# Kernel optimization log

Measured on AMD Instinct MI355X. Metric: run time of the kernel, lower is better.

The kernel has to match this reference:

```python
import jax, jax.numpy as jnp
import numpy as np

H = 1024      # hidden_size
V = 50257     # output_size (vocab)
L = 12        # max_length


def setup_inputs() -> dict:
    key = jax.random.key(0)
    ks = jax.random.split(key, 16)
    s = 0.02  # weight init scale
    return {
        "input_tok": jax.random.randint(ks[0], (1,), 0, V, dtype=jnp.int64) if jax.config.read('jax_enable_x64') else jax.random.randint(ks[0], (1,), 0, V, dtype=jnp.int32),
        "hidden": jax.random.normal(ks[1], (1, 1, H), jnp.float32),
        "encoder_outputs": jax.random.normal(ks[2], (L, H), jnp.float32),
        "emb": jax.random.normal(ks[3], (V, H), jnp.float32) * s,
        "attn_W": jax.random.normal(ks[4], (L, 2 * H), jnp.float32) * s,
        "attn_b": jnp.zeros((L,), jnp.float32),
        "comb_W": jax.random.normal(ks[5], (H, 2 * H), jnp.float32) * s,
        "comb_b": jnp.zeros((H,), jnp.float32),
        "Wih": jax.random.normal(ks[6], (H, H), jnp.float32) * s,
        "Whh": jax.random.normal(ks[7], (H, H), jnp.float32) * s,
        "bih": jnp.zeros((H,), jnp.float32),
        "bhh": jnp.zeros((H,), jnp.float32),
        "out_W": jax.random.normal(ks[8], (V, H), jnp.float32) * s,
        "out_b": jnp.zeros((V,), jnp.float32),
    }


def reference(input_tok, hidden, encoder_outputs, emb, attn_W, attn_b,
              comb_W, comb_b, Wih, Whh, bih, bhh, out_W, out_b):
    # embedding lookup -> [1, H]  (dropout = identity in eval mode)
    embedded = emb[input_tok[0]][None, :]
    h0 = hidden[0]  # [1, H]
    # Bahdanau-style attention over encoder_outputs [L, H]
    attn_in = jnp.concatenate([embedded, h0], axis=1)           # [1, 2H]
    attn_weights = jax.nn.softmax(attn_in @ attn_W.T + attn_b, axis=1)  # [1, L]
    attn_applied = attn_weights @ encoder_outputs               # [1, H]
    # combine + relu
    x = jnp.concatenate([embedded, attn_applied], axis=1)       # [1, 2H]
    x = jax.nn.relu(x @ comb_W.T + comb_b)                      # [1, H]
    # single vanilla-RNN (tanh) step
    h_new = jnp.tanh(x @ Wih.T + bih + h0 @ Whh.T + bhh)        # [1, H]
    # output projection + log_softmax over vocab
    logp = jax.nn.log_softmax(h_new @ out_W.T + out_b, axis=1)  # [1, V]
    return logp, h_new[None, :, :], attn_weights
```

## Files before the change

kernel.cpp:

```cpp
#include <hip/hip_runtime.h>
#include <math.h>

#define H 1024
#define V 50257
#define L 12

#define OFF_EMB    0
#define OFF_ATTN   1024
#define OFF_X      2048
#define OFF_H0     3072
#define OFF_H      4096
#define OFF_LOGITS 5120
#define OFF_PART   56384
#define NB4        4096

__device__ __forceinline__ float dot4(float4 a, float4 b) {
    return a.x * b.x + a.y * b.y + a.z * b.z + a.w * b.w;
}

__device__ __forceinline__ float wave_red(float s) {
    for (int o = 32; o > 0; o >>= 1) s += __shfl_down(s, o);
    return s;
}

__global__ __launch_bounds__(1024) void k1_attn(
    const int* __restrict__ tok_p, const float* __restrict__ hidden,
    const float* __restrict__ enc, const float* __restrict__ emb,
    const float* __restrict__ attn_W, const float* __restrict__ attn_b,
    float* __restrict__ ws, float* __restrict__ out)
{
    __shared__ float4 att_in4[512];
    __shared__ float wsm[L];
    float* att_in = (float*)att_in4;
    const int t = threadIdx.x;
    const int wave = t >> 6;
    const int lane = t & 63;
    const int tok = tok_p[0];

    float e  = emb[(size_t)tok * H + t];
    float h0 = hidden[t];
    att_in[t]       = e;
    att_in[H + t]   = h0;
    ws[OFF_EMB + t] = e;
    ws[OFF_H0 + t]  = h0;
    __syncthreads();

    if (wave < L) {
        const float4* wr = (const float4*)(attn_W + (size_t)wave * 2 * H);
        float s = 0.f;
#pragma unroll
        for (int i = 0; i < 8; ++i)
            s += dot4(wr[lane + 64 * i], att_in4[lane + 64 * i]);
        s = wave_red(s);
        if (lane == 0) wsm[wave] = s + attn_b[wave];
    }
    __syncthreads();

    if (t == 0) {
        float m = wsm[0];
        for (int l = 1; l < L; ++l) m = fmaxf(m, wsm[l]);
        float s = 0.f;
        for (int l = 0; l < L; ++l) { wsm[l] = expf(wsm[l] - m); s += wsm[l]; }
        float inv = 1.f / s;
        for (int l = 0; l < L; ++l) {
            wsm[l] *= inv;
            out[V + H + l] = wsm[l];
        }
    }
    __syncthreads();

    float a = 0.f;
#pragma unroll
    for (int l = 0; l < L; ++l) a += wsm[l] * enc[l * H + t];
    ws[OFF_ATTN + t] = a;
}

__global__ __launch_bounds__(256) void k2_combine(
    const float* __restrict__ comb_W, const float* __restrict__ comb_b,
    float* __restrict__ ws)
{
    const int wave = threadIdx.x >> 6;
    const int lane = threadIdx.x & 63;
    const int row = blockIdx.x * 4 + wave;
    const float4* Wr = (const float4*)(comb_W + (size_t)row * 2 * H);
    const float4* vv = (const float4*)(ws + OFF_EMB);
    float s = 0.f;
#pragma unroll
    for (int i = 0; i < 8; ++i)
        s += dot4(Wr[lane + 64 * i], vv[lane + 64 * i]);
    s = wave_red(s);
    if (lane == 0) ws[OFF_X + row] = fmaxf(s + comb_b[row], 0.f);
}

__global__ __launch_bounds__(256) void k3_rnn(
    const float* __restrict__ Wih, const float* __restrict__ Whh,
    const float* __restrict__ bih, const float* __restrict__ bhh,
    float* __restrict__ ws, float* __restrict__ out)
{
    const int wave = threadIdx.x >> 6;
    const int lane = threadIdx.x & 63;
    const int row = blockIdx.x * 4 + wave;
    const float4* Wi = (const float4*)(Wih + (size_t)row * H);
    const float4* Wh = (const float4*)(Whh + (size_t)row * H);
    const float4* xv = (const float4*)(ws + OFF_X);
    const float4* hv = (const float4*)(ws + OFF_H0);
    float s = 0.f;
#pragma unroll
    for (int i = 0; i < 4; ++i)
        s += dot4(Wi[lane + 64 * i], xv[lane + 64 * i])
           + dot4(Wh[lane + 64 * i], hv[lane + 64 * i]);
    s = wave_red(s);
    if (lane == 0) {
        float h = tanhf(s + bih[row] + bhh[row]);
        ws[OFF_H + row] = h;
        out[V + row] = h;
    }
}

__global__ __launch_bounds__(256) void k4_outproj(
    const float* __restrict__ out_W, const float* __restrict__ out_b,
    float* __restrict__ ws)
{
    __shared__ float red[4];
    const int wave = threadIdx.x >> 6;
    const int lane = threadIdx.x & 63;
    const float4* hv = (const float4*)(ws + OFF_H);
    const float4 h0 = hv[lane];
    const float4 h1 = hv[lane + 64];
    const float4 h2 = hv[lane + 128];
    const float4 h3 = hv[lane + 192];
    float esum = 0.f;
    for (int row = blockIdx.x * 4 + wave; row < V; row += NB4 * 4) {
        const float4* Wr = (const float4*)(out_W + (size_t)row * H);
        float s = dot4(Wr[lane], h0) + dot4(Wr[lane + 64], h1)
                + dot4(Wr[lane + 128], h2) + dot4(Wr[lane + 192], h3);
        s = wave_red(s);
        if (lane == 0) {
            float d = s + out_b[row];
            ws[OFF_LOGITS + row] = d;
            esum += expf(d);
        }
    }
    if (lane == 0) red[wave] = esum;
    __syncthreads();
    if (threadIdx.x == 0)
        ws[OFF_PART + blockIdx.x] = red[0] + red[1] + red[2] + red[3];
}

__global__ __launch_bounds__(256) void k5_norm(
    const float* __restrict__ ws, float* __restrict__ out)
{
    __shared__ float red[4];
    __shared__ float sbc;
    const int t = threadIdx.x;
    const int wave = t >> 6;
    const int lane = t & 63;
    float s = 0.f;
    for (int i = t; i < NB4; i += 256) s += ws[OFF_PART + i];
    s = wave_red(s);
    if (lane == 0) red[wave] = s;
    __syncthreads();
    if (t == 0) sbc = logf(red[0] + red[1] + red[2] + red[3]);
    __syncthreads();
    const float lse = sbc;
    const int idx = blockIdx.x * 256 + t;
    if (idx < V) out[idx] = ws[OFF_LOGITS + idx] - lse;
}

extern "C" void kernel_launch(void* const* d_in, const int* in_sizes, int n_in,
                              void* d_out, int out_size, void* d_ws, size_t ws_size,
                              hipStream_t stream) {
    const int*   tok    = (const int*)d_in[0];
    const float* hidden = (const float*)d_in[1];
    const float* enc    = (const float*)d_in[2];
    const float* emb    = (const float*)d_in[3];
    const float* attn_W = (const float*)d_in[4];
    const float* attn_b = (const float*)d_in[5];
    const float* comb_W = (const float*)d_in[6];
    const float* comb_b = (const float*)d_in[7];
    const float* Wih    = (const float*)d_in[8];
    const float* Whh    = (const float*)d_in[9];
    const float* bih    = (const float*)d_in[10];
    const float* bhh    = (const float*)d_in[11];
    const float* out_W  = (const float*)d_in[12];
    const float* out_b  = (const float*)d_in[13];
    float* ws  = (float*)d_ws;
    float* out = (float*)d_out;

    k1_attn   <<<1,                1024, 0, stream>>>(tok, hidden, enc, emb, attn_W, attn_b, ws, out);
    k2_combine<<<H / 4,            256,  0, stream>>>(comb_W, comb_b, ws);
    k3_rnn    <<<H / 4,            256,  0, stream>>>(Wih, Whh, bih, bhh, ws, out);
    k4_outproj<<<NB4,              256,  0, stream>>>(out_W, out_b, ws);
    k5_norm   <<<(V + 255) / 256,  256,  0, stream>>>(ws, out);
}
```

Before: 407.0 us.

## Hoist Whh·h0 matvec into attention kernel and give one row per wave in outproj

The recurrent Whh·h0 product depends only on the input hidden state, so it moves into the first kernel as 64 extra blocks that run alongside the single attention block. The RNN kernel then only streams Wih, which halves its memory traffic on the critical path. The output projection drops its grid-stride loop and launches one row per wave (12565 blocks), so k5 must now reduce many more partial sums. The wider first kernel adds little cost, but the extra blocks and the larger partial-sum reduction add some overhead.

After: 407.9 us. Within noise of the previous version (+0.2%).

```diff
diff --git a/kernel.cpp b/kernel.cpp
--- a/kernel.cpp
+++ b/kernel.cpp
@@ -10,9 +10,10 @@
 #define OFF_X      2048
 #define OFF_H0     3072
 #define OFF_H      4096
-#define OFF_LOGITS 5120
-#define OFF_PART   56384
-#define NB4        4096
+#define OFF_HH     5120
+#define OFF_LOGITS 6144
+#define OFF_PART   56448
+#define NB4        12565
 
 __device__ __forceinline__ float dot4(float4 a, float4 b) {
     return a.x * b.x + a.y * b.y + a.z * b.z + a.w * b.w;
@@ -27,14 +28,27 @@
     const int* __restrict__ tok_p, const float* __restrict__ hidden,
     const float* __restrict__ enc, const float* __restrict__ emb,
     const float* __restrict__ attn_W, const float* __restrict__ attn_b,
+    const float* __restrict__ Whh, const float* __restrict__ bhh,
     float* __restrict__ ws, float* __restrict__ out)
 {
+    const int t = threadIdx.x;
+    const int wave = t >> 6;
+    const int lane = t & 63;
+
+    if (blockIdx.x != 0) {
+        const int row = (blockIdx.x - 1) * 16 + wave;
+        const float4* Wh = (const float4*)(Whh + (size_t)row * H);
+        const float4* hv = (const float4*)hidden;
+        float s = dot4(Wh[lane], hv[lane]) + dot4(Wh[lane + 64], hv[lane + 64])
+                + dot4(Wh[lane + 128], hv[lane + 128]) + dot4(Wh[lane + 192], hv[lane + 192]);
+        s = wave_red(s);
+        if (lane == 0) ws[OFF_HH + row] = s + bhh[row];
+        return;
+    }
+
     __shared__ float4 att_in4[512];
     __shared__ float wsm[L];
     float* att_in = (float*)att_in4;
-    const int t = threadIdx.x;
-    const int wave = t >> 6;
-    const int lane = t & 63;
     const int tok = tok_p[0];
 
     float e  = emb[(size_t)tok * H + t];
@@ -93,25 +107,19 @@
 }
 
 __global__ __launch_bounds__(256) void k3_rnn(
-    const float* __restrict__ Wih, const float* __restrict__ Whh,
-    const float* __restrict__ bih, const float* __restrict__ bhh,
+    const float* __restrict__ Wih, const float* __restrict__ bih,
     float* __restrict__ ws, float* __restrict__ out)
 {
     const int wave = threadIdx.x >> 6;
     const int lane = threadIdx.x & 63;
     const int row = blockIdx.x * 4 + wave;
     const float4* Wi = (const float4*)(Wih + (size_t)row * H);
-    const float4* Wh = (const float4*)(Whh + (size_t)row * H);
     const float4* xv = (const float4*)(ws + OFF_X);
-    const float4* hv = (const float4*)(ws + OFF_H0);
-    float s = 0.f;
-#pragma unroll
-    for (int i = 0; i < 4; ++i)
-        s += dot4(Wi[lane + 64 * i], xv[lane + 64 * i])
-           + dot4(Wh[lane + 64 * i], hv[lane + 64 * i]);
+    float s = dot4(Wi[lane], xv[lane]) + dot4(Wi[lane + 64], xv[lane + 64])
+            + dot4(Wi[lane + 128], xv[lane + 128]) + dot4(Wi[lane + 192], xv[lane + 192]);
     s = wave_red(s);
     if (lane == 0) {
-        float h = tanhf(s + bih[row] + bhh[row]);
+        float h = tanhf(s + bih[row] + ws[OFF_HH + row]);
         ws[OFF_H + row] = h;
         out[V + row] = h;
     }
@@ -124,24 +132,21 @@
     __shared__ float red[4];
     const int wave = threadIdx.x >> 6;
     const int lane = threadIdx.x & 63;
+    const int row = blockIdx.x * 4 + wave;
     const float4* hv = (const float4*)(ws + OFF_H);
-    const float4 h0 = hv[lane];
-    const float4 h1 = hv[lane + 64];
-    const float4 h2 = hv[lane + 128];
-    const float4 h3 = hv[lane + 192];
-    float esum = 0.f;
-    for (int row = blockIdx.x * 4 + wave; row < V; row += NB4 * 4) {
+    float e = 0.f;
+    if (row < V) {
         const float4* Wr = (const float4*)(out_W + (size_t)row * H);
-        float s = dot4(Wr[lane], h0) + dot4(Wr[lane + 64], h1)
-                + dot4(Wr[lane + 128], h2) + dot4(Wr[lane + 192], h3);
+        float s = dot4(Wr[lane], hv[lane]) + dot4(Wr[lane + 64], hv[lane + 64])
+                + dot4(Wr[lane + 128], hv[lane + 128]) + dot4(Wr[lane + 192], hv[lane + 192]);
         s = wave_red(s);
         if (lane == 0) {
             float d = s + out_b[row];
             ws[OFF_LOGITS + row] = d;
-            esum += expf(d);
+            e = expf(d);
         }
     }
-    if (lane == 0) red[wave] = esum;
+    if (lane == 0) red[wave] = e;
     __syncthreads();
     if (threadIdx.x == 0)
         ws[OFF_PART + blockIdx.x] = red[0] + red[1] + red[2] + red[3];
@@ -187,9 +192,10 @@
     float* ws  = (float*)d_ws;
     float* out = (float*)d_out;
 
-    k1_attn   <<<1,                1024, 0, stream>>>(tok, hidden, enc, emb, attn_W, attn_b, ws, out);
+    k1_attn   <<<65,               1024, 0, stream>>>(tok, hidden, enc, emb, attn_W, attn_b,
+                                                      Whh, bhh, ws, out);
     k2_combine<<<H / 4,            256,  0, stream>>>(comb_W, comb_b, ws);
-    k3_rnn    <<<H / 4,            256,  0, stream>>>(Wih, Whh, bih, bhh, ws, out);
+    k3_rnn    <<<H / 4,            256,  0, stream>>>(Wih, bih, ws, out);
     k4_outproj<<<NB4,              256,  0, stream>>>(out_W, out_b, ws);
     k5_norm   <<<(V + 255) / 256,  256,  0, stream>>>(ws, out);
 }
```
